# Optimization experiments

Hardware: AMD Instinct MI355X
Metric: run time of the kernel (lower is better)

Reference implementation:

```python
import jax, jax.numpy as jnp
import numpy as np

N_NODES = 20000
N_EDGES = 320000
IN_CH = 256
HID_CH = 512


def setup_inputs() -> dict:
    key = jax.random.key(0)
    k_x, k_e, k_w1, k_w2 = jax.random.split(key, 4)
    x = jax.random.normal(k_x, (N_NODES, IN_CH), dtype=jnp.float32)
    edge_index = jax.random.randint(k_e, (2, N_EDGES), 0, N_NODES, dtype=jnp.int32)
    # Glorot-style init for the two GCNConv weight matrices; PyG GCNConv bias init is zeros.
    W1 = jax.random.normal(k_w1, (IN_CH, HID_CH), dtype=jnp.float32) * (1.0 / np.sqrt(IN_CH))
    b1 = jnp.zeros((HID_CH,), dtype=jnp.float32)
    W2 = jax.random.normal(k_w2, (HID_CH, HID_CH), dtype=jnp.float32) * (1.0 / np.sqrt(HID_CH))
    b2 = jnp.zeros((HID_CH,), dtype=jnp.float32)
    return {"x": x, "edge_index": edge_index, "W1": W1, "b1": b1, "W2": W2, "b2": b2}


def _gcn_conv(x, W, b, src, dst, n_nodes):
    """PyG GCNConv: linear transform, then sym-normalized aggregation with self-loops."""
    h = x @ W  # [N, H]
    # in-degree on dst, +1 for the implicit self-loop
    deg = jnp.zeros((n_nodes,), dtype=h.dtype).at[dst].add(1.0) + 1.0
    dinv = jax.lax.rsqrt(deg)  # deg >= 1 always
    norm = dinv[src] * dinv[dst]  # [E]
    msg = h[src] * norm[:, None]  # [E, H] gathered, normalized messages
    agg = jax.ops.segment_sum(msg, dst, num_segments=n_nodes)  # scatter-add to targets
    # self-loop contribution: norm for edge i->i is dinv[i]^2
    return agg + h * (dinv * dinv)[:, None] + b


def reference(x, edge_index, W1, b1, W2, b2):
    src, dst = edge_index[0], edge_index[1]
    n = x.shape[0]
    h = jax.nn.relu(_gcn_conv(x, W1, b1, src, dst, n))
    # dropout(p=0.2) is identity in eval mode
    return _gcn_conv(h, W2, b2, src, dst, n)
```

## Files before the change

### kernel.cpp

```cpp
#include <hip/hip_runtime.h>

#define N_NODES 20000
#define N_EDGES 320000
#define IN_CH 256
#define HID_CH 512
#define NB_SCAN ((N_NODES + 255) / 256)

typedef unsigned short u16;
typedef __attribute__((ext_vector_type(4))) float f32x4;
typedef __attribute__((ext_vector_type(8))) short bf16x8;
typedef __attribute__((ext_vector_type(4))) u16 u16x4;
typedef __attribute__((ext_vector_type(8))) u16 u16x8;

__device__ __forceinline__ float bf2f(u16 h) { return __uint_as_float((unsigned)h << 16); }
__device__ __forceinline__ u16 f2bf(float f) {
    unsigned u = __float_as_uint(f);
    return (u16)((u + 0x7fffu + ((u >> 16) & 1u)) >> 16);
}

__global__ void zero2_kernel(int* __restrict__ a, int* __restrict__ b, int n) {
    int i = blockIdx.x * blockDim.x + threadIdx.x;
    if (i < n) { a[i] = 0; b[i] = 0; }
}

__global__ void count_deg_kernel(const int* __restrict__ dst, int* __restrict__ deg, int E) {
    int i = blockIdx.x * blockDim.x + threadIdx.x;
    if (i < E) atomicAdd(&deg[dst[i]], 1);
}

__global__ __launch_bounds__(256) void scan_pass1(const int* __restrict__ deg,
                                                  float* __restrict__ dinv,
                                                  int* __restrict__ bsum, int N) {
    __shared__ int tmp[256];
    int t = threadIdx.x;
    int i = blockIdx.x * 256 + t;
    int d = (i < N) ? deg[i] : 0;
    if (i < N) dinv[i] = rsqrtf((float)d + 1.0f);
    tmp[t] = d;
    __syncthreads();
#pragma unroll
    for (int off = 128; off > 0; off >>= 1) {
        if (t < off) tmp[t] += tmp[t + off];
        __syncthreads();
    }
    if (t == 0) bsum[blockIdx.x] = tmp[0];
}

__global__ __launch_bounds__(128) void scan_pass2(int* __restrict__ bsum, int NB) {
    __shared__ int tmp[128];
    int t = threadIdx.x;
    tmp[t] = (t < NB) ? bsum[t] : 0;
    __syncthreads();
#pragma unroll
    for (int off = 1; off < 128; off <<= 1) {
        int v = (t >= off) ? tmp[t - off] : 0;
        __syncthreads();
        tmp[t] += v;
        __syncthreads();
    }
    if (t < NB) bsum[t] = (t == 0) ? 0 : tmp[t - 1];
}

__global__ __launch_bounds__(256) void scan_pass3(const int* __restrict__ deg,
                                                  const int* __restrict__ bsum,
                                                  int* __restrict__ row_ptr, int N, int E) {
    __shared__ int tmp[256];
    int t = threadIdx.x;
    int i = blockIdx.x * 256 + t;
    int d = (i < N) ? deg[i] : 0;
    tmp[t] = d;
    __syncthreads();
#pragma unroll
    for (int off = 1; off < 256; off <<= 1) {
        int v = (t >= off) ? tmp[t - off] : 0;
        __syncthreads();
        tmp[t] += v;
        __syncthreads();
    }
    if (i < N) row_ptr[i] = bsum[blockIdx.x] + tmp[t] - d;
    if (i == 0) row_ptr[N] = E;
}

__global__ void scatter_edges_kernel(const int* __restrict__ src, const int* __restrict__ dst,
                                     const int* __restrict__ row_ptr, int* __restrict__ cursor,
                                     const float* __restrict__ dinv, int2* __restrict__ epair,
                                     int E) {
    int e = blockIdx.x * blockDim.x + threadIdx.x;
    if (e >= E) return;
    int d = dst[e];
    int s = src[e];
    int pos = row_ptr[d] + atomicAdd(&cursor[d], 1);
    epair[pos] = make_int2(s, __float_as_int(dinv[s]));
}

__global__ void f32_to_bf16_kernel(const float* __restrict__ in, u16* __restrict__ out, int n4) {
    int i = blockIdx.x * blockDim.x + threadIdx.x;
    if (i >= n4) return;
    float4 v = ((const float4*)in)[i];
    u16x4 o = {f2bf(v.x), f2bf(v.y), f2bf(v.z), f2bf(v.w)};
    ((u16x4*)out)[i] = o;
}

__global__ __launch_bounds__(256) void convert_w_kernel(const float* __restrict__ W1,
                                                        u16* __restrict__ hi1, u16* __restrict__ lo1,
                                                        const float* __restrict__ W2,
                                                        u16* __restrict__ hi2, u16* __restrict__ lo2) {
    __shared__ float t[64][65];
    int b = blockIdx.x;
    const float* W;
    u16 *hi, *lo;
    int K;
    if (b < 32) { W = W1; hi = hi1; lo = lo1; K = IN_CH; }
    else        { b -= 32; W = W2; hi = hi2; lo = lo2; K = HID_CH; }
    const int N = HID_CH;
    int k0 = (b >> 3) * 64, n0 = (b & 7) * 64;
    int c = threadIdx.x & 63, r4 = threadIdx.x >> 6;
#pragma unroll
    for (int i = 0; i < 16; ++i) {
        int r = i * 4 + r4;
        t[r][c] = W[(size_t)(k0 + r) * N + n0 + c];
    }
    __syncthreads();
#pragma unroll
    for (int i = 0; i < 16; ++i) {
        int n = i * 4 + r4;
        float f = t[c][n];
        u16 hb = f2bf(f);
        size_t o = (size_t)(n0 + n) * K + k0 + c;
        hi[o] = hb;
        lo[o] = f2bf(f - bf2f(hb));
    }
}

template <int C, int SLICES>
__global__ __launch_bounds__(256) void gather_agg_kernel(
        const u16* __restrict__ h, const int2* __restrict__ epair,
        const int* __restrict__ row_ptr, const float* __restrict__ dinv,
        u16* __restrict__ z, int N) {
    int bid = blockIdx.x;
    int nb, s;
    if (SLICES == 8) {
        nb = bid >> 3;
        s = bid & 7;
    } else {
        nb = (bid >> 3) * 2 + (bid & 1);
        s = (bid & 7) >> 1;
    }
    int t = threadIdx.x;
    int grp = t >> 3;
    int u = t & 7;
    int n = nb * 32 + grp;
    bool alive = (n < N);
    int nn = alive ? n : (N - 1);
    float dn = dinv[nn];
    const u16* hbase = h + s * 64 + u * 8;
    float acc[8];
    {
        u16x8 ws = *(const u16x8*)(hbase + (size_t)nn * C);
        float sf = dn * dn;
#pragma unroll
        for (int j = 0; j < 8; ++j) acc[j] = bf2f(ws[j]) * sf;
    }
    int e0 = row_ptr[nn];
    int e1 = alive ? row_ptr[nn + 1] : e0;
    int e = e0;
    for (; e + 4 <= e1; e += 4) {
        int2 p0 = epair[e + 0], p1 = epair[e + 1], p2 = epair[e + 2], p3 = epair[e + 3];
        u16x8 w0 = *(const u16x8*)(hbase + (size_t)p0.x * C);
        u16x8 w1 = *(const u16x8*)(hbase + (size_t)p1.x * C);
        u16x8 w2 = *(const u16x8*)(hbase + (size_t)p2.x * C);
        u16x8 w3 = *(const u16x8*)(hbase + (size_t)p3.x * C);
        float n0 = __int_as_float(p0.y) * dn, n1 = __int_as_float(p1.y) * dn;
        float n2 = __int_as_float(p2.y) * dn, n3 = __int_as_float(p3.y) * dn;
#pragma unroll
        for (int j = 0; j < 8; ++j) {
            acc[j] = fmaf(bf2f(w0[j]), n0, acc[j]);
            acc[j] = fmaf(bf2f(w1[j]), n1, acc[j]);
            acc[j] = fmaf(bf2f(w2[j]), n2, acc[j]);
            acc[j] = fmaf(bf2f(w3[j]), n3, acc[j]);
        }
    }
    for (; e < e1; ++e) {
        int2 p = epair[e];
        u16x8 w = *(const u16x8*)(hbase + (size_t)p.x * C);
        float nr = __int_as_float(p.y) * dn;
#pragma unroll
        for (int j = 0; j < 8; ++j) acc[j] = fmaf(bf2f(w[j]), nr, acc[j]);
    }
    if (alive) {
        u16x8 vh;
#pragma unroll
        for (int j = 0; j < 8; ++j) vh[j] = f2bf(acc[j]);
        *(u16x8*)(z + (size_t)n * C + s * 64 + u * 8) = vh;
    }
}

template <int K, bool RELU, bool OUT_BF16>
__global__ __launch_bounds__(512, 6) void gemm_mfma_kernel(
        const u16* __restrict__ A, const u16* __restrict__ Bh, const u16* __restrict__ Bl,
        const float* __restrict__ bias, void* __restrict__ Cout, int M, int N) {
    __shared__ u16 lds[2][12288];
    const int tid = threadIdx.x;
    const int lane = tid & 63;
    const int wid = tid >> 6;

    const int nmt = (M + 127) / 128;
    const int total = nmt * 4;
    int bid = blockIdx.x;
    int q = total >> 3, r = total & 7;
    int xcd = bid & 7, pp = bid >> 3;
    int lin = (xcd < r) ? (xcd * (q + 1) + pp) : (r * (q + 1) + (xcd - r) * q + pp);
    const int bm = (lin >> 2) * 128;
    const int bn = (lin & 3) * 128;

    const int wm = (wid & 1) * 64;
    const int wn = (wid >> 1) * 32;

    f32x4 acc[4][2];
#pragma unroll
    for (int i = 0; i < 4; ++i)
#pragma unroll
        for (int j = 0; j < 2; ++j) acc[i][j] = (f32x4){0.f, 0.f, 0.f, 0.f};

    const int srow = (wid << 4) + (lane >> 2);
    const int scb = (((lane & 3) ^ ((lane >> 3) & 3)) << 4);
    const char* srcA  = (const char*)(A  + (size_t)min(bm + srow, M - 1) * K) + scb;
    const char* srcBh = (const char*)(Bh + (size_t)(bn + srow) * K) + scb;
    const char* srcBl = (const char*)(Bl + (size_t)(bn + srow) * K) + scb;
    const int dstoff = wid << 10;

#define GLL(srcp, dstb)                                                                  \
    __builtin_amdgcn_global_load_lds(                                                    \
        (const __attribute__((address_space(1))) void*)(srcp),                           \
        (__attribute__((address_space(3))) void*)((char*)&lds[buf][0] + (dstb)), 16, 0, 0)

#define STAGE(bufv, k0)                                                                  \
    do {                                                                                 \
        int buf = (bufv);                                                                \
        size_t kb2 = (size_t)(k0) * 2;                                                   \
        GLL(srcA + kb2, dstoff);                                                         \
        GLL(srcBh + kb2, 8192 + dstoff);                                                 \
        GLL(srcBl + kb2, 16384 + dstoff);                                                \
    } while (0)

    STAGE(0, 0);

    const int NT = K / 32;
    const int kb = (lane >> 4) << 4;
#pragma unroll
    for (int t = 0; t < NT; ++t) {
        int cur = t & 1;
        if (t + 1 < NT) {
            STAGE(cur ^ 1, (t + 1) * 32);
            asm volatile("s_waitcnt vmcnt(3)" ::: "memory");
        } else {
            asm volatile("s_waitcnt vmcnt(0)" ::: "memory");
        }
        __builtin_amdgcn_s_barrier();
        asm volatile("" ::: "memory");

        const char* L = (const char*)&lds[cur][0];
        bf16x8 a[4], b_h[2], b_l[2];
#pragma unroll
        for (int i = 0; i < 4; ++i) {
            int ra = wm + i * 16 + (lane & 15);
            int off = ra * 64 + (kb ^ (((ra >> 1) & 3) << 4));
            a[i] = *(const bf16x8*)(L + off);
        }
#pragma unroll
        for (int j = 0; j < 2; ++j) {
            int rb = wn + j * 16 + (lane & 15);
            int off = rb * 64 + (kb ^ (((rb >> 1) & 3) << 4));
            b_h[j] = *(const bf16x8*)(L + 8192 + off);
            b_l[j] = *(const bf16x8*)(L + 16384 + off);
        }
#pragma unroll
        for (int i = 0; i < 4; ++i)
#pragma unroll
            for (int j = 0; j < 2; ++j) {
                acc[i][j] = __builtin_amdgcn_mfma_f32_16x16x32_bf16(a[i], b_h[j], acc[i][j], 0, 0, 0);
                acc[i][j] = __builtin_amdgcn_mfma_f32_16x16x32_bf16(a[i], b_l[j], acc[i][j], 0, 0, 0);
            }
        asm volatile("" ::: "memory");
        __builtin_amdgcn_s_barrier();
    }
#undef STAGE
#undef GLL

#pragma unroll
    for (int j = 0; j < 2; ++j) {
        int gc = bn + wn + j * 16 + (lane & 15);
        float bv = bias[gc];
#pragma unroll
        for (int i = 0; i < 4; ++i) {
#pragma unroll
            for (int t = 0; t < 4; ++t) {
                int gr = bm + wm + i * 16 + ((lane >> 4) << 2) + t;
                if (gr < M) {
                    float v = acc[i][j][t] + bv;
                    if (RELU) v = fmaxf(v, 0.f);
                    if (OUT_BF16)
                        ((u16*)Cout)[(size_t)gr * N + gc] = f2bf(v);
                    else
                        ((float*)Cout)[(size_t)gr * N + gc] = v;
                }
            }
        }
    }
}

extern "C" void kernel_launch(void* const* d_in, const int* in_sizes, int n_in,
                              void* d_out, int out_size, void* d_ws, size_t ws_size,
                              hipStream_t stream) {
    const float* x  = (const float*)d_in[0];
    const int*   ei = (const int*)d_in[1];
    const float* W1 = (const float*)d_in[2];
    const float* b1 = (const float*)d_in[3];
    const float* W2 = (const float*)d_in[4];
    const float* b2 = (const float*)d_in[5];
    const int* src = ei;
    const int* dst = ei + N_EDGES;

    char* ws = (char*)d_ws;
    size_t off = 0;
    auto alloc = [&](size_t bytes) {
        void* p = ws + off;
        off = (off + bytes + 255) & ~(size_t)255;
        return p;
    };
    int*   deg     = (int*)alloc(N_NODES * 4);
    int*   cursor  = (int*)alloc(N_NODES * 4);
    int*   row_ptr = (int*)alloc((N_NODES + 1) * 4);
    float* dinv    = (float*)alloc(N_NODES * 4);
    int*   bsum    = (int*)alloc(NB_SCAN * 4);
    int2*  epair   = (int2*)alloc((size_t)N_EDGES * 8);
    u16*   wt1_hi  = (u16*)alloc((size_t)IN_CH * HID_CH * 2);
    u16*   wt1_lo  = (u16*)alloc((size_t)IN_CH * HID_CH * 2);
    u16*   wt2_hi  = (u16*)alloc((size_t)HID_CH * HID_CH * 2);
    u16*   wt2_lo  = (u16*)alloc((size_t)HID_CH * HID_CH * 2);
    u16*   xb      = (u16*)alloc((size_t)N_NODES * IN_CH * 2);
    u16*   z1      = (u16*)alloc((size_t)N_NODES * IN_CH * 2);
    u16*   z2      = (u16*)alloc((size_t)N_NODES * HID_CH * 2);
    u16*   h1      = (u16*)d_out;

    zero2_kernel<<<NB_SCAN, 256, 0, stream>>>(deg, cursor, N_NODES);
    count_deg_kernel<<<(N_EDGES + 255) / 256, 256, 0, stream>>>(dst, deg, N_EDGES);
    scan_pass1<<<NB_SCAN, 256, 0, stream>>>(deg, dinv, bsum, N_NODES);
    scan_pass2<<<1, 128, 0, stream>>>(bsum, NB_SCAN);
    scan_pass3<<<NB_SCAN, 256, 0, stream>>>(deg, bsum, row_ptr, N_NODES, N_EDGES);
    scatter_edges_kernel<<<(N_EDGES + 255) / 256, 256, 0, stream>>>(src, dst, row_ptr, cursor,
                                                                    dinv, epair, N_EDGES);

    f32_to_bf16_kernel<<<(N_NODES * IN_CH / 4 + 255) / 256, 256, 0, stream>>>(
        x, xb, N_NODES * IN_CH / 4);
    convert_w_kernel<<<96, 256, 0, stream>>>(W1, wt1_hi, wt1_lo, W2, wt2_hi, wt2_lo);

    const int NMT = (N_NODES + 127) / 128;
    const int NB32 = (N_NODES + 31) / 32;
    gather_agg_kernel<IN_CH, 4><<<((NB32 + 1) / 2) * 8, 256, 0, stream>>>(
        xb, epair, row_ptr, dinv, z1, N_NODES);
    gemm_mfma_kernel<IN_CH, true, true><<<NMT * 4, 512, 0, stream>>>(
        z1, wt1_hi, wt1_lo, b1, h1, N_NODES, HID_CH);

    gather_agg_kernel<HID_CH, 8><<<NB32 * 8, 256, 0, stream>>>(
        h1, epair, row_ptr, dinv, z2, N_NODES);
    gemm_mfma_kernel<HID_CH, false, false><<<NMT * 4, 512, 0, stream>>>(
        z2, wt2_hi, wt2_lo, b2, (float*)d_out, N_NODES, HID_CH);
}
```

Baseline: 158.3 us.

## Merge prep kernels, fold scan pass2, drop low-bf16 term in layer-1 GEMM

```diff
diff --git a/kernel.cpp b/kernel.cpp
--- a/kernel.cpp
+++ b/kernel.cpp
@@ -18,9 +18,51 @@
     return (u16)((u + 0x7fffu + ((u >> 16) & 1u)) >> 16);
 }
 
-__global__ void zero2_kernel(int* __restrict__ a, int* __restrict__ b, int n) {
-    int i = blockIdx.x * blockDim.x + threadIdx.x;
-    if (i < n) { a[i] = 0; b[i] = 0; }
+__global__ __launch_bounds__(256) void prep_kernel(
+        int* __restrict__ deg, int* __restrict__ cursor,
+        const float* __restrict__ x, u16* __restrict__ xb,
+        const float* __restrict__ W1, u16* __restrict__ hi1, u16* __restrict__ lo1,
+        const float* __restrict__ W2, u16* __restrict__ hi2, u16* __restrict__ lo2) {
+    __shared__ float t[64][65];
+    int b = blockIdx.x;
+    if (b < NB_SCAN) {
+        int i = b * 256 + threadIdx.x;
+        if (i < N_NODES) { deg[i] = 0; cursor[i] = 0; }
+        return;
+    }
+    b -= NB_SCAN;
+    const int XB = N_NODES * IN_CH / 4 / 256;
+    if (b < XB) {
+        int i = b * 256 + threadIdx.x;
+        float4 v = ((const float4*)x)[i];
+        u16x4 o = {f2bf(v.x), f2bf(v.y), f2bf(v.z), f2bf(v.w)};
+        ((u16x4*)xb)[i] = o;
+        return;
+    }
+    b -= XB;
+    const float* W;
+    u16 *hi, *lo;
+    int K;
+    if (b < 32) { W = W1; hi = hi1; lo = lo1; K = IN_CH; }
+    else        { b -= 32; W = W2; hi = hi2; lo = lo2; K = HID_CH; }
+    const int N = HID_CH;
+    int k0 = (b >> 3) * 64, n0 = (b & 7) * 64;
+    int c = threadIdx.x & 63, r4 = threadIdx.x >> 6;
+#pragma unroll
+    for (int i = 0; i < 16; ++i) {
+        int r = i * 4 + r4;
+        t[r][c] = W[(size_t)(k0 + r) * N + n0 + c];
+    }
+    __syncthreads();
+#pragma unroll
+    for (int i = 0; i < 16; ++i) {
+        int n = i * 4 + r4;
+        float f = t[c][n];
+        u16 hb = f2bf(f);
+        size_t o = (size_t)(n0 + n) * K + k0 + c;
+        hi[o] = hb;
+        lo[o] = f2bf(f - bf2f(hb));
+    }
 }
 
 __global__ void count_deg_kernel(const int* __restrict__ dst, int* __restrict__ deg, int E) {
@@ -46,26 +88,22 @@
     if (t == 0) bsum[blockIdx.x] = tmp[0];
 }
 
-__global__ __launch_bounds__(128) void scan_pass2(int* __restrict__ bsum, int NB) {
-    __shared__ int tmp[128];
-    int t = threadIdx.x;
-    tmp[t] = (t < NB) ? bsum[t] : 0;
-    __syncthreads();
-#pragma unroll
-    for (int off = 1; off < 128; off <<= 1) {
-        int v = (t >= off) ? tmp[t - off] : 0;
-        __syncthreads();
-        tmp[t] += v;
-        __syncthreads();
-    }
-    if (t < NB) bsum[t] = (t == 0) ? 0 : tmp[t - 1];
-}
-
 __global__ __launch_bounds__(256) void scan_pass3(const int* __restrict__ deg,
                                                   const int* __restrict__ bsum,
                                                   int* __restrict__ row_ptr, int N, int E) {
     __shared__ int tmp[256];
+    __shared__ int bs[128];
     int t = threadIdx.x;
+    if (t < 128) bs[t] = (t < NB_SCAN) ? bsum[t] : 0;
+    __syncthreads();
+#pragma unroll
+    for (int off = 1; off < 128; off <<= 1) {
+        int v = (t >= off && t < 128) ? bs[t - off] : 0;
+        __syncthreads();
+        if (t < 128) bs[t] += v;
+        __syncthreads();
+    }
+    int base = (blockIdx.x == 0) ? 0 : bs[blockIdx.x - 1];
     int i = blockIdx.x * 256 + t;
     int d = (i < N) ? deg[i] : 0;
     tmp[t] = d;
@@ -77,7 +115,7 @@
         tmp[t] += v;
         __syncthreads();
     }
-    if (i < N) row_ptr[i] = bsum[blockIdx.x] + tmp[t] - d;
+    if (i < N) row_ptr[i] = base + tmp[t] - d;
     if (i == 0) row_ptr[N] = E;
 }
 
@@ -91,45 +129,6 @@
     int s = src[e];
     int pos = row_ptr[d] + atomicAdd(&cursor[d], 1);
     epair[pos] = make_int2(s, __float_as_int(dinv[s]));
-}
-
-__global__ void f32_to_bf16_kernel(const float* __restrict__ in, u16* __restrict__ out, int n4) {
-    int i = blockIdx.x * blockDim.x + threadIdx.x;
-    if (i >= n4) return;
-    float4 v = ((const float4*)in)[i];
-    u16x4 o = {f2bf(v.x), f2bf(v.y), f2bf(v.z), f2bf(v.w)};
-    ((u16x4*)out)[i] = o;
-}
-
-__global__ __launch_bounds__(256) void convert_w_kernel(const float* __restrict__ W1,
-                                                        u16* __restrict__ hi1, u16* __restrict__ lo1,
-                                                        const float* __restrict__ W2,
-                                                        u16* __restrict__ hi2, u16* __restrict__ lo2) {
-    __shared__ float t[64][65];
-    int b = blockIdx.x;
-    const float* W;
-    u16 *hi, *lo;
-    int K;
-    if (b < 32) { W = W1; hi = hi1; lo = lo1; K = IN_CH; }
-    else        { b -= 32; W = W2; hi = hi2; lo = lo2; K = HID_CH; }
-    const int N = HID_CH;
-    int k0 = (b >> 3) * 64, n0 = (b & 7) * 64;
-    int c = threadIdx.x & 63, r4 = threadIdx.x >> 6;
-#pragma unroll
-    for (int i = 0; i < 16; ++i) {
-        int r = i * 4 + r4;
-        t[r][c] = W[(size_t)(k0 + r) * N + n0 + c];
-    }
-    __syncthreads();
-#pragma unroll
-    for (int i = 0; i < 16; ++i) {
-        int n = i * 4 + r4;
-        float f = t[c][n];
-        u16 hb = f2bf(f);
-        size_t o = (size_t)(n0 + n) * K + k0 + c;
-        hi[o] = hb;
-        lo[o] = f2bf(f - bf2f(hb));
-    }
 }
 
 template <int C, int SLICES>
@@ -195,11 +194,11 @@
     }
 }
 
-template <int K, bool RELU, bool OUT_BF16>
-__global__ __launch_bounds__(512, 6) void gemm_mfma_kernel(
+template <int K, bool RELU, bool OUT_BF16, bool TWO_TERM>
+__global__ __launch_bounds__(512, TWO_TERM ? 6 : 8) void gemm_mfma_kernel(
         const u16* __restrict__ A, const u16* __restrict__ Bh, const u16* __restrict__ Bl,
         const float* __restrict__ bias, void* __restrict__ Cout, int M, int N) {
-    __shared__ u16 lds[2][12288];
+    __shared__ u16 lds[2][TWO_TERM ? 12288 : 8192];
     const int tid = threadIdx.x;
     const int lane = tid & 63;
     const int wid = tid >> 6;
@@ -240,7 +239,7 @@
         size_t kb2 = (size_t)(k0) * 2;                                                   \
         GLL(srcA + kb2, dstoff);                                                         \
         GLL(srcBh + kb2, 8192 + dstoff);                                                 \
-        GLL(srcBl + kb2, 16384 + dstoff);                                                \
+        if (TWO_TERM) GLL(srcBl + kb2, 16384 + dstoff);                                  \
     } while (0)
 
     STAGE(0, 0);
@@ -252,7 +251,10 @@
         int cur = t & 1;
         if (t + 1 < NT) {
             STAGE(cur ^ 1, (t + 1) * 32);
-            asm volatile("s_waitcnt vmcnt(3)" ::: "memory");
+            if constexpr (TWO_TERM)
+                asm volatile("s_waitcnt vmcnt(3)" ::: "memory");
+            else
+                asm volatile("s_waitcnt vmcnt(2)" ::: "memory");
         } else {
             asm volatile("s_waitcnt vmcnt(0)" ::: "memory");
         }
@@ -272,14 +274,15 @@
             int rb = wn + j * 16 + (lane & 15);
             int off = rb * 64 + (kb ^ (((rb >> 1) & 3) << 4));
             b_h[j] = *(const bf16x8*)(L + 8192 + off);
-            b_l[j] = *(const bf16x8*)(L + 16384 + off);
+            if (TWO_TERM) b_l[j] = *(const bf16x8*)(L + 16384 + off);
         }
 #pragma unroll
         for (int i = 0; i < 4; ++i)
 #pragma unroll
             for (int j = 0; j < 2; ++j) {
                 acc[i][j] = __builtin_amdgcn_mfma_f32_16x16x32_bf16(a[i], b_h[j], acc[i][j], 0, 0, 0);
-                acc[i][j] = __builtin_amdgcn_mfma_f32_16x16x32_bf16(a[i], b_l[j], acc[i][j], 0, 0, 0);
+                if (TWO_TERM)
+                    acc[i][j] = __builtin_amdgcn_mfma_f32_16x16x32_bf16(a[i], b_l[j], acc[i][j], 0, 0, 0);
             }
         asm volatile("" ::: "memory");
         __builtin_amdgcn_s_barrier();
@@ -343,27 +346,24 @@
     u16*   z2      = (u16*)alloc((size_t)N_NODES * HID_CH * 2);
     u16*   h1      = (u16*)d_out;
 
-    zero2_kernel<<<NB_SCAN, 256, 0, stream>>>(deg, cursor, N_NODES);
+    const int XB = N_NODES * IN_CH / 4 / 256;
+    prep_kernel<<<NB_SCAN + XB + 96, 256, 0, stream>>>(deg, cursor, x, xb, W1, wt1_hi, wt1_lo,
+                                                       W2, wt2_hi, wt2_lo);
     count_deg_kernel<<<(N_EDGES + 255) / 256, 256, 0, stream>>>(dst, deg, N_EDGES);
     scan_pass1<<<NB_SCAN, 256, 0, stream>>>(deg, dinv, bsum, N_NODES);
-    scan_pass2<<<1, 128, 0, stream>>>(bsum, NB_SCAN);
     scan_pass3<<<NB_SCAN, 256, 0, stream>>>(deg, bsum, row_ptr, N_NODES, N_EDGES);
     scatter_edges_kernel<<<(N_EDGES + 255) / 256, 256, 0, stream>>>(src, dst, row_ptr, cursor,
                                                                     dinv, epair, N_EDGES);
-
-    f32_to_bf16_kernel<<<(N_NODES * IN_CH / 4 + 255) / 256, 256, 0, stream>>>(
-        x, xb, N_NODES * IN_CH / 4);
-    convert_w_kernel<<<96, 256, 0, stream>>>(W1, wt1_hi, wt1_lo, W2, wt2_hi, wt2_lo);
 
     const int NMT = (N_NODES + 127) / 128;
     const int NB32 = (N_NODES + 31) / 32;
     gather_agg_kernel<IN_CH, 4><<<((NB32 + 1) / 2) * 8, 256, 0, stream>>>(
         xb, epair, row_ptr, dinv, z1, N_NODES);
-    gemm_mfma_kernel<IN_CH, true, true><<<NMT * 4, 512, 0, stream>>>(
+    gemm_mfma_kernel<IN_CH, true, true, false><<<NMT * 4, 512, 0, stream>>>(
         z1, wt1_hi, wt1_lo, b1, h1, N_NODES, HID_CH);
 
     gather_agg_kernel<HID_CH, 8><<<NB32 * 8, 256, 0, stream>>>(
         h1, epair, row_ptr, dinv, z2, N_NODES);
-    gemm_mfma_kernel<HID_CH, false, false><<<NMT * 4, 512, 0, stream>>>(
+    gemm_mfma_kernel<HID_CH, false, false, true><<<NMT * 4, 512, 0, stream>>>(
         z2, wt2_hi, wt2_lo, b2, (float*)d_out, N_NODES, HID_CH);
 }
```

Result: faster. 146.6 us (-7.4%).
